# Optimization experiments

Measured on AMD Instinct MI355X. Metric: run time of the kernel, lower is better.

## Reference

```python
import jax, jax.numpy as jnp
import numpy as np

D = 2048
N = 4096
HEAD = 2
DH = D // HEAD


def setup_inputs() -> dict:
    key = jax.random.key(0)
    ks = jax.random.split(key, 7)
    s = 0.02  # realistic init scale for weights
    x = jax.random.normal(ks[0], (1, N, D), jnp.float32)
    Wq1 = jax.random.normal(ks[1], (DH, DH), jnp.float32) * s
    Wq2 = jax.random.normal(ks[2], (DH, DH), jnp.float32) * s
    Wk1 = jax.random.normal(ks[3], (DH, DH), jnp.float32) * s
    Wk2 = jax.random.normal(ks[4], (DH, DH), jnp.float32) * s
    Wv1 = jax.random.normal(ks[5], (DH, DH), jnp.float32) * s
    Wv2 = jax.random.normal(ks[6], (DH, DH), jnp.float32) * s
    return {"x": x, "Wq1": Wq1, "Wq2": Wq2, "Wk1": Wk1, "Wk2": Wk2,
            "Wv1": Wv1, "Wv2": Wv2}


def _head(xh, Wq, Wk, Wv):
    # xh: [1, N, Dh]; Linear applies in @ W^T (no bias)
    q = (xh @ Wq.T)[0]                      # [N, Dh]
    k = (xh @ Wk.T)[0]                      # [N, Dh] (k reshaped to 2D in torch)
    v = (xh @ Wv.T)[0]                      # [N, Dh]
    # QK_T linear with weight dynamically set to k (detached in torch):
    Sc = q @ jax.lax.stop_gradient(k).T     # [N, N]
    # Sc_V linear on v^T with weight set to Sc (detached in torch):
    Sc = jax.lax.stop_gradient(Sc)
    return v.T @ Sc.T                       # [Dh, N]  == (Sc @ v)^T


def reference(x, Wq1, Wq2, Wk1, Wk2, Wv1, Wv2):
    Dh = Wq1.shape[0]
    x1, x2 = x[..., :Dh], x[..., Dh:]       # torch.chunk(x, 2, dim=2)
    o1 = _head(x1, Wq1, Wk1, Wv1)           # [Dh, N]
    o2 = _head(x2, Wq2, Wk2, Wv2)           # [Dh, N]
    out = jnp.concatenate([o1, o2], axis=0).T  # transpose(-2,-1).squeeze -> [N, D]
    return out
```

## Files before the change

kernel.cpp:

```cpp
#include <hip/hip_runtime.h>
#include <hip/hip_bf16.h>


using bf16 = __hip_bfloat16;
typedef __attribute__((ext_vector_type(8))) __bf16 bf16x8;
typedef __attribute__((ext_vector_type(8))) unsigned short u16x8;
typedef __attribute__((ext_vector_type(4))) float f32x4;

#define M1 (1024 * 1024)

struct GB {
    const bf16* A[20];
    const bf16* B[20];
    void*       C[20];
    int lda[20];
    int ldb[20];
};

__device__ __forceinline__ void gload_lds16(const void* g, void* l) {
    __builtin_amdgcn_global_load_lds(
        (const __attribute__((address_space(1))) void*)g,
        (__attribute__((address_space(3))) void*)l, 16, 0, 0);
}

template<int N>
__device__ __forceinline__ void waitv() {
    if constexpr (N == 4)      asm volatile("s_waitcnt vmcnt(4)" ::: "memory");
    else if constexpr (N == 3) asm volatile("s_waitcnt vmcnt(3)" ::: "memory");
    else                       asm volatile("s_waitcnt vmcnt(0)" ::: "memory");
}

template<int BM_, int BN_, typename OUT_T>
__global__ __launch_bounds__(256, 4)
void gemm_bt_pa(GB g, int Ksub, int ldc)
{
    const int gx = gridDim.x, gy = gridDim.y;
    const int nwg = gx * gy * gridDim.z;
    const int orig = blockIdx.x + gx * (blockIdx.y + gy * blockIdx.z);
    const int cpx = nwg >> 3;
    const int wg = (orig & 7) * cpx + (orig >> 3);
    const int bx = wg % gx;
    const int by = (wg / gx) % gy;
    const int bz = wg / (gx * gy);

    const bf16* __restrict__ A = g.A[bz];
    const bf16* __restrict__ B = g.B[bz];
    OUT_T* __restrict__ C = (OUT_T*)g.C[bz];
    const int lda = g.lda[bz];
    const int ldb = g.ldb[bz];

    constexpr int STAGE_SH = 2 * (BM_ + BN_) * 32;
    constexpr int EPI_SH   = BM_ * BN_ * (int)sizeof(OUT_T) / 2;
    constexpr int SMEM_SH  = STAGE_SH > EPI_SH ? STAGE_SH : EPI_SH;
    __shared__ __align__(16) unsigned short smem[SMEM_SH];
    auto As = (unsigned short(*)[BM_ * 32])smem;
    auto Bs = (unsigned short(*)[BN_ * 32])(smem + 2 * BM_ * 32);

    constexpr int MI = BM_ / 32;
    constexpr int NI = BN_ / 32;
    constexpr int NLOADS = (BM_ + BN_) / 64;

    const int tid  = threadIdx.x;
    const int lane = tid & 63;
    const int wave = tid >> 6;
    const int wm   = wave >> 1;
    const int wn   = wave & 1;

    const int m0 = by * BM_;
    const int n0 = bx * BN_;

    const int fr = lane & 15;
    const int kg = lane >> 4;

    const int srow = tid >> 2;
    const int scol = (tid & 3) * 8;

    auto stage = [&](int buf, int kt) {
        #pragma unroll
        for (int r = 0; r < BM_ / 64; ++r)
            gload_lds16(A + (size_t)(m0 + r * 64 + srow) * lda + (kt + scol),
                        &As[buf][(r * 64 + srow) * 32 + scol]);
        #pragma unroll
        for (int r = 0; r < BN_ / 64; ++r)
            gload_lds16(B + (size_t)(n0 + r * 64 + srow) * ldb + (kt + scol),
                        &Bs[buf][(r * 64 + srow) * 32 + scol]);
    };

    f32x4 acc[MI][NI];
    #pragma unroll
    for (int i = 0; i < MI; ++i)
        #pragma unroll
        for (int j = 0; j < NI; ++j)
            acc[i][j] = {0.f, 0.f, 0.f, 0.f};

    const int niter = Ksub >> 5;
    int cur = 0;
    stage(0, 0);

    for (int it = 0; it < niter; ++it) {
        if (it + 1 < niter) {
            stage(cur ^ 1, (it + 1) << 5);
            waitv<NLOADS>();
        } else {
            waitv<0>();
        }
        __builtin_amdgcn_s_barrier();
        __builtin_amdgcn_sched_barrier(0);

        bf16x8 afrag[MI], bfrag[NI];
        #pragma unroll
        for (int mi = 0; mi < MI; ++mi)
            afrag[mi] = *(const bf16x8*)&As[cur][(wm * (BM_ / 2) + mi * 16 + fr) * 32 + kg * 8];
        #pragma unroll
        for (int ni = 0; ni < NI; ++ni)
            bfrag[ni] = *(const bf16x8*)&Bs[cur][(wn * (BN_ / 2) + ni * 16 + fr) * 32 + kg * 8];

        #pragma unroll
        for (int mi = 0; mi < MI; ++mi)
            #pragma unroll
            for (int ni = 0; ni < NI; ++ni)
                acc[mi][ni] = __builtin_amdgcn_mfma_f32_16x16x32_bf16(
                    afrag[mi], bfrag[ni], acc[mi][ni], 0, 0, 0);

        __builtin_amdgcn_sched_barrier(0);
        __builtin_amdgcn_s_barrier();
        __builtin_amdgcn_sched_barrier(0);
        cur ^= 1;
    }

    if constexpr (sizeof(OUT_T) == 2) {
        #pragma unroll
        for (int mi = 0; mi < MI; ++mi)
            #pragma unroll
            for (int ni = 0; ni < NI; ++ni) {
                const int c = wn * (BN_ / 2) + ni * 16 + fr;
                #pragma unroll
                for (int j = 0; j < 4; ++j) {
                    const int r = wm * (BM_ / 2) + mi * 16 + kg * 4 + j;
                    bf16 h = __float2bfloat16(acc[mi][ni][j]);
                    smem[r * BN_ + c] = *(unsigned short*)&h;
                }
            }
        __syncthreads();
        constexpr int V = (BM_ * BN_) / 2048;
        #pragma unroll
        for (int v = 0; v < V; ++v) {
            const int off = v * 2048 + tid * 8;
            const int r = off / BN_;
            const int c = off % BN_;
            *(u16x8*)((unsigned short*)C + (size_t)(m0 + r) * ldc + n0 + c) =
                *(const u16x8*)&smem[off];
        }
    } else {
        float* fs = (float*)smem;
        #pragma unroll
        for (int mi = 0; mi < MI; ++mi)
            #pragma unroll
            for (int ni = 0; ni < NI; ++ni) {
                const int c = wn * (BN_ / 2) + ni * 16 + fr;
                #pragma unroll
                for (int j = 0; j < 4; ++j) {
                    const int r = wm * (BM_ / 2) + mi * 16 + kg * 4 + j;
                    fs[r * BN_ + c] = acc[mi][ni][j];
                }
            }
        __syncthreads();
        constexpr int V = (BM_ * BN_) / 1024;
        #pragma unroll
        for (int v = 0; v < V; ++v) {
            const int off = v * 1024 + tid * 4;
            const int r = off / BN_;
            const int c = off % BN_;
            *(float4*)((float*)C + (size_t)(m0 + r) * ldc + n0 + c) =
                *(const float4*)&fs[off];
        }
    }
}


__device__ __forceinline__ ushort4 cvt4(float4 v) {
    ushort4 o; bf16 h;
    h = __float2bfloat16(v.x); o.x = *(unsigned short*)&h;
    h = __float2bfloat16(v.y); o.y = *(unsigned short*)&h;
    h = __float2bfloat16(v.z); o.z = *(unsigned short*)&h;
    h = __float2bfloat16(v.w); o.w = *(unsigned short*)&h;
    return o;
}

struct PrepArgs {
    const float* x;
    const float* w[4];
    const float* wv[2];
    bf16* xb;
    bf16* xt;
    bf16* wdst;
};

__device__ void xpose64(const float* __restrict__ src, int ldsrc,
                        int r0, int c0,
                        bf16* __restrict__ dstS, int ldS,
                        bf16* __restrict__ dstT, int ldT,
                        float (*tile)[65], int t)
{
    const int tr  = t >> 4;
    const int tc4 = (t & 15) * 4;
    #pragma unroll
    for (int ph = 0; ph < 4; ++ph) {
        const int row = ph * 16 + tr;
        float4 v = *(const float4*)(src + (size_t)(r0 + row) * ldsrc + c0 + tc4);
        tile[row][tc4 + 0] = v.x;
        tile[row][tc4 + 1] = v.y;
        tile[row][tc4 + 2] = v.z;
        tile[row][tc4 + 3] = v.w;
        if (dstS)
            *(ushort4*)((unsigned short*)dstS + (size_t)(r0 + row) * ldS + c0 + tc4) = cvt4(v);
    }
    __syncthreads();
    #pragma unroll
    for (int ph = 0; ph < 4; ++ph) {
        const int crow = ph * 16 + tr;
        float4 v = {tile[tc4 + 0][crow], tile[tc4 + 1][crow],
                    tile[tc4 + 2][crow], tile[tc4 + 3][crow]};
        *(ushort4*)((unsigned short*)dstT + (size_t)(c0 + crow) * ldT + r0 + tc4) = cvt4(v);
    }
}

__global__ void prep(PrepArgs p)
{
    __shared__ float tile[64][65];
    const int b = blockIdx.x;
    const int t = threadIdx.x;

    if (b < 2048) {
        const int n0 = (b & 63) * 64;
        const int c0 = (b >> 6) * 64;
        xpose64(p.x, 2048, n0, c0, p.xb, 2048, p.xt, 4096, tile, t);
    } else if (b < 3072) {
        const int i = b - 2048;
        const int mat = i >> 8;
        const int tl  = i & 255;
        const int r0 = (tl & 15) * 64;
        const int c0 = (tl >> 4) * 64;
        xpose64(p.w[mat], 1024, r0, c0, nullptr, 0,
                p.wdst + (size_t)mat * M1, 1024, tile, t);
    } else {
        const int i = b - 3072;
        const int mat = i >> 9;
        const int blk = i & 511;
        const size_t off = (size_t)blk * 2048 + t * 8;
        float4 v0 = *(const float4*)(p.wv[mat] + off);
        float4 v1 = *(const float4*)(p.wv[mat] + off + 4);
        unsigned short* d = (unsigned short*)p.wdst + (size_t)(4 + mat) * M1 + off;
        *(ushort4*)d       = cvt4(v0);
        *(ushort4*)(d + 4) = cvt4(v1);
    }
}


__device__ __forceinline__ void reduce_slices(const unsigned short* src,
                                              unsigned short* dst,
                                              int h, int r, int nslice)
{
    float acc[8] = {0, 0, 0, 0, 0, 0, 0, 0};
    for (int s = 0; s < nslice; ++s) {
        u16x8 v = *(const u16x8*)(src + ((size_t)(h * nslice + s) << 20) + r);
        #pragma unroll
        for (int j = 0; j < 8; ++j)
            acc[j] += __uint_as_float(((unsigned)v[j]) << 16);
    }
    u16x8 o;
    #pragma unroll
    for (int j = 0; j < 8; ++j) {
        bf16 hh = __float2bfloat16(acc[j]);
        o[j] = *(unsigned short*)&hh;
    }
    *(u16x8*)(dst + ((size_t)h << 20) + r) = o;
}

__global__ void reduce_GM(const unsigned short* Gp, const unsigned short* Mp,
                          unsigned short* Gd, unsigned short* Md)
{
    const int b = blockIdx.x, t = threadIdx.x;
    if (b < 1024) {
        const int e = (b * 256 + t) * 8;
        reduce_slices(Gp, Gd, e >> 20, e & (M1 - 1), 8);
    } else {
        const int e = ((b - 1024) * 256 + t) * 8;
        reduce_slices(Mp, Md, e >> 20, e & (M1 - 1), 2);
    }
}

__global__ void reduce_4(const unsigned short* Sp, unsigned short* Dd)
{
    const int e = (blockIdx.x * 256 + threadIdx.x) * 8;
    reduce_slices(Sp, Dd, e >> 20, e & (M1 - 1), 4);
}


extern "C" void kernel_launch(void* const* d_in, const int* in_sizes, int n_in,
                              void* d_out, int out_size, void* d_ws, size_t ws_size,
                              hipStream_t stream)
{
    bf16* xb   = (bf16*)d_ws;
    bf16* xt   = xb + 8 * M1;
    bf16* wdst = xt + 8 * M1;
    bf16* Mp   = wdst + 6 * M1;
    bf16* Mb   = Mp + 4 * M1;
    bf16* Gb   = Mb + 2 * M1;
    bf16* Ytb  = Gb + 2 * M1;
    bf16* Utb  = Ytb + 2 * M1;

    bf16* scr = (bf16*)d_out;

    PrepArgs pa;
    pa.x = (const float*)d_in[0];
    pa.w[0] = (const float*)d_in[1];  pa.w[1] = (const float*)d_in[2];
    pa.w[2] = (const float*)d_in[3];  pa.w[3] = (const float*)d_in[4];
    pa.wv[0] = (const float*)d_in[5]; pa.wv[1] = (const float*)d_in[6];
    pa.xb = xb; pa.xt = xt; pa.wdst = wdst;
    prep<<<4096, 256, 0, stream>>>(pa);

    GB g;

    for (int z = 0; z < 16; ++z) {
        const int h = z >> 3, s = z & 7;
        g.A[z] = xt + (size_t)h * 4 * M1 + s * 512;  g.lda[z] = 4096;
        g.B[z] = g.A[z];                             g.ldb[z] = 4096;
        g.C[z] = (bf16*)scr + (size_t)z * M1;
    }
    for (int z = 16; z < 20; ++z) {
        const int j = z - 16, h = j >> 1, s = j & 1;
        g.A[z] = wdst + (size_t)h * M1 + s * 512;           g.lda[z] = 1024;
        g.B[z] = wdst + (size_t)(2 + h) * M1 + s * 512;     g.ldb[z] = 1024;
        g.C[z] = Mp + (size_t)j * M1;
    }
    gemm_bt_pa<128, 128, bf16><<<dim3(8, 8, 20), 256, 0, stream>>>(g, 512, 1024);

    reduce_GM<<<2048, 256, 0, stream>>>((const unsigned short*)scr, (const unsigned short*)Mp,
                                        (unsigned short*)Gb, (unsigned short*)Mb);

    for (int z = 0; z < 8; ++z) {
        const int h = z >> 2, s = z & 3;
        g.A[z] = Mb + (size_t)h * M1 + s * 256;  g.lda[z] = 1024;
        g.B[z] = Gb + (size_t)h * M1 + s * 256;  g.ldb[z] = 1024;
        g.C[z] = (bf16*)scr + (size_t)z * M1;
    }
    gemm_bt_pa<128, 128, bf16><<<dim3(8, 8, 8), 256, 0, stream>>>(g, 256, 1024);

    reduce_4<<<1024, 256, 0, stream>>>((const unsigned short*)scr, (unsigned short*)Ytb);

    for (int z = 0; z < 8; ++z) {
        const int h = z >> 2, s = z & 3;
        g.A[z] = wdst + (size_t)(4 + h) * M1 + s * 256;  g.lda[z] = 1024;
        g.B[z] = Ytb + (size_t)h * M1 + s * 256;         g.ldb[z] = 1024;
        g.C[z] = (bf16*)scr + (size_t)z * M1;
    }
    gemm_bt_pa<128, 128, bf16><<<dim3(8, 8, 8), 256, 0, stream>>>(g, 256, 1024);

    reduce_4<<<1024, 256, 0, stream>>>((const unsigned short*)scr, (unsigned short*)Utb);

    for (int z = 0; z < 2; ++z) {
        g.A[z] = xb + (size_t)z * 1024;   g.lda[z] = 2048;
        g.B[z] = Utb + (size_t)z * M1;    g.ldb[z] = 1024;
        g.C[z] = (float*)d_out + (size_t)z * 1024;
    }
    gemm_bt_pa<128, 64, float><<<dim3(16, 32, 2), 256, 0, stream>>>(g, 1024, 2048);
}
```

Measured before the change: 124.3 us.

## Compute only upper-triangular tiles of symmetric Gram matrix and mirror in reduction

The Gram matrix G = X^T X per head is symmetric, so the first batched GEMM now computes only the 36 upper-triangular 128x128 tiles per split-K slice instead of all 64. The Wq·Wk product tiles are packed into the same launch as a second branch. The reduction kernel sums the compact tile slices and writes each off-diagonal tile twice, once transposed, which removes close to half of the Gram GEMM work and partial-sum traffic. In exchange, the mirrored writes are scattered element stores with poor coalescing, and the triangle index is decoded with a small loop.

```diff
diff --git a/kernel.cpp b/kernel.cpp
--- a/kernel.cpp
+++ b/kernel.cpp
@@ -10,11 +10,11 @@
 #define M1 (1024 * 1024)
 
 struct GB {
-    const bf16* A[20];
-    const bf16* B[20];
-    void*       C[20];
-    int lda[20];
-    int ldb[20];
+    const bf16* A[8];
+    const bf16* B[8];
+    void*       C[8];
+    int lda[8];
+    int ldb[8];
 };
 
 __device__ __forceinline__ void gload_lds16(const void* g, void* l) {
@@ -31,28 +31,13 @@
 }
 
 template<int BM_, int BN_, typename OUT_T>
-__global__ __launch_bounds__(256, 4)
-void gemm_bt_pa(GB g, int Ksub, int ldc)
-{
-    const int gx = gridDim.x, gy = gridDim.y;
-    const int nwg = gx * gy * gridDim.z;
-    const int orig = blockIdx.x + gx * (blockIdx.y + gy * blockIdx.z);
-    const int cpx = nwg >> 3;
-    const int wg = (orig & 7) * cpx + (orig >> 3);
-    const int bx = wg % gx;
-    const int by = (wg / gx) % gy;
-    const int bz = wg / (gx * gy);
-
-    const bf16* __restrict__ A = g.A[bz];
-    const bf16* __restrict__ B = g.B[bz];
-    OUT_T* __restrict__ C = (OUT_T*)g.C[bz];
-    const int lda = g.lda[bz];
-    const int ldb = g.ldb[bz];
-
-    constexpr int STAGE_SH = 2 * (BM_ + BN_) * 32;
-    constexpr int EPI_SH   = BM_ * BN_ * (int)sizeof(OUT_T) / 2;
-    constexpr int SMEM_SH  = STAGE_SH > EPI_SH ? STAGE_SH : EPI_SH;
-    __shared__ __align__(16) unsigned short smem[SMEM_SH];
+__device__ __forceinline__ void gemm_core(
+    const bf16* __restrict__ A, int lda,
+    const bf16* __restrict__ B, int ldb,
+    OUT_T* __restrict__ C, int ldc,
+    int m0, int n0, int Ksub,
+    unsigned short* smem, int tid)
+{
     auto As = (unsigned short(*)[BM_ * 32])smem;
     auto Bs = (unsigned short(*)[BN_ * 32])(smem + 2 * BM_ * 32);
 
@@ -60,18 +45,12 @@
     constexpr int NI = BN_ / 32;
     constexpr int NLOADS = (BM_ + BN_) / 64;
 
-    const int tid  = threadIdx.x;
     const int lane = tid & 63;
     const int wave = tid >> 6;
     const int wm   = wave >> 1;
     const int wn   = wave & 1;
-
-    const int m0 = by * BM_;
-    const int n0 = bx * BN_;
-
     const int fr = lane & 15;
     const int kg = lane >> 4;
-
     const int srow = tid >> 2;
     const int scol = (tid & 3) * 8;
 
@@ -174,6 +153,73 @@
             *(float4*)((float*)C + (size_t)(m0 + r) * ldc + n0 + c) =
                 *(const float4*)&fs[off];
         }
+    }
+}
+
+template<int BM_, int BN_, typename OUT_T>
+__global__ __launch_bounds__(256, 4)
+void gemm_bt_pa(GB g, int Ksub, int ldc)
+{
+    constexpr int STAGE_SH = 2 * (BM_ + BN_) * 32;
+    constexpr int EPI_SH   = BM_ * BN_ * (int)sizeof(OUT_T) / 2;
+    constexpr int SMEM_SH  = STAGE_SH > EPI_SH ? STAGE_SH : EPI_SH;
+    __shared__ __align__(16) unsigned short smem[SMEM_SH];
+
+    const int gx = gridDim.x, gy = gridDim.y;
+    const int nwg = gx * gy * gridDim.z;
+    const int orig = blockIdx.x + gx * (blockIdx.y + gy * blockIdx.z);
+    const int cpx = nwg >> 3;
+    const int wg = (orig & 7) * cpx + (orig >> 3);
+    const int bx = wg % gx;
+    const int by = (wg / gx) % gy;
+    const int bz = wg / (gx * gy);
+
+    gemm_core<BM_, BN_, OUT_T>(g.A[bz], g.lda[bz], g.B[bz], g.ldb[bz],
+                               (OUT_T*)g.C[bz], ldc,
+                               by * BM_, bx * BN_, Ksub,
+                               smem, threadIdx.x);
+}
+
+struct B1Args {
+    const bf16* xt;
+    const bf16* wdst;
+    bf16* Gp;
+    bf16* Mp;
+};
+
+__global__ __launch_bounds__(256, 4)
+void b1_kernel(B1Args a)
+{
+    __shared__ __align__(16) unsigned short smem[16384];
+
+    const int nwg = 832;
+    const int orig = blockIdx.x + 52 * blockIdx.z;
+    const int cpx = nwg >> 3;
+    const int wg = (orig & 7) * cpx + (orig >> 3);
+    const int bx = wg % 52;
+    const int bz = wg / 52;
+
+    if (bx < 36) {
+        const int h = bz >> 3, s = bz & 7;
+        int ti = 0, rem = bx;
+        while (rem >= 8 - ti) { rem -= 8 - ti; ++ti; }
+        const int tj = ti + rem;
+        const bf16* A = a.xt + (size_t)(h * 1024 + ti * 128) * 4096 + s * 512;
+        const bf16* B = a.xt + (size_t)(h * 1024 + tj * 128) * 4096 + s * 512;
+        bf16* C = a.Gp + ((size_t)bz * 36 + bx) * 16384;
+        gemm_core<128, 128, bf16>(A, 4096, B, 4096, C, 128, 0, 0, 512,
+                                  smem, threadIdx.x);
+    } else {
+        const int combo = bz & 3;
+        const int h = combo >> 1, s = combo & 1;
+        const int tile = (bz >> 2) * 16 + (bx - 36);
+        const int m0 = (tile >> 3) * 128;
+        const int n0 = (tile & 7) * 128;
+        const bf16* A = a.wdst + (size_t)h * M1 + s * 512;
+        const bf16* B = a.wdst + (size_t)(2 + h) * M1 + s * 512;
+        bf16* C = a.Mp + (size_t)combo * M1;
+        gemm_core<128, 128, bf16>(A, 1024, B, 1024, C, 1024, m0, n0, 512,
+                                  smem, threadIdx.x);
     }
 }
 
@@ -281,11 +327,41 @@
                           unsigned short* Gd, unsigned short* Md)
 {
     const int b = blockIdx.x, t = threadIdx.x;
-    if (b < 1024) {
-        const int e = (b * 256 + t) * 8;
-        reduce_slices(Gp, Gd, e >> 20, e & (M1 - 1), 8);
+    if (b < 576) {
+        const int h    = b / 288;
+        const int rem  = b - h * 288;
+        const int tile = rem >> 3;
+        const int blk  = rem & 7;
+        int ti = 0, trem = tile;
+        while (trem >= 8 - ti) { trem -= 8 - ti; ++ti; }
+        const int tj = ti + trem;
+
+        const int e  = blk * 2048 + t * 8;
+        const int r  = e >> 7;
+        const int c0 = e & 127;
+
+        float acc[8] = {0, 0, 0, 0, 0, 0, 0, 0};
+        for (int s = 0; s < 8; ++s) {
+            u16x8 v = *(const u16x8*)(Gp + ((size_t)(h * 8 + s) * 36 + tile) * 16384 + e);
+            #pragma unroll
+            for (int j = 0; j < 8; ++j)
+                acc[j] += __uint_as_float(((unsigned)v[j]) << 16);
+        }
+        u16x8 o;
+        #pragma unroll
+        for (int j = 0; j < 8; ++j) {
+            bf16 hh = __float2bfloat16(acc[j]);
+            o[j] = *(unsigned short*)&hh;
+        }
+        unsigned short* G = Gd + (size_t)h * M1;
+        *(u16x8*)(G + (size_t)(ti * 128 + r) * 1024 + tj * 128 + c0) = o;
+        if (ti != tj) {
+            #pragma unroll
+            for (int j = 0; j < 8; ++j)
+                G[(size_t)(tj * 128 + c0 + j) * 1024 + ti * 128 + r] = o[j];
+        }
     } else {
-        const int e = ((b - 1024) * 256 + t) * 8;
+        const int e = ((b - 576) * 256 + t) * 8;
         reduce_slices(Mp, Md, e >> 20, e & (M1 - 1), 2);
     }
 }
@@ -320,24 +396,15 @@
     pa.xb = xb; pa.xt = xt; pa.wdst = wdst;
     prep<<<4096, 256, 0, stream>>>(pa);
 
+    B1Args b1;
+    b1.xt = xt; b1.wdst = wdst; b1.Gp = scr; b1.Mp = Mp;
+    b1_kernel<<<dim3(52, 1, 16), 256, 0, stream>>>(b1);
+
+    reduce_GM<<<1600, 256, 0, stream>>>((const unsigned short*)scr,
+                                        (const unsigned short*)Mp,
+                                        (unsigned short*)Gb, (unsigned short*)Mb);
+
     GB g;
-
-    for (int z = 0; z < 16; ++z) {
-        const int h = z >> 3, s = z & 7;
-        g.A[z] = xt + (size_t)h * 4 * M1 + s * 512;  g.lda[z] = 4096;
-        g.B[z] = g.A[z];                             g.ldb[z] = 4096;
-        g.C[z] = (bf16*)scr + (size_t)z * M1;
-    }
-    for (int z = 16; z < 20; ++z) {
-        const int j = z - 16, h = j >> 1, s = j & 1;
-        g.A[z] = wdst + (size_t)h * M1 + s * 512;           g.lda[z] = 1024;
-        g.B[z] = wdst + (size_t)(2 + h) * M1 + s * 512;     g.ldb[z] = 1024;
-        g.C[z] = Mp + (size_t)j * M1;
-    }
-    gemm_bt_pa<128, 128, bf16><<<dim3(8, 8, 20), 256, 0, stream>>>(g, 512, 1024);
-
-    reduce_GM<<<2048, 256, 0, stream>>>((const unsigned short*)scr, (const unsigned short*)Mp,
-                                        (unsigned short*)Gb, (unsigned short*)Mb);
 
     for (int z = 0; z < 8; ++z) {
         const int h = z >> 2, s = z & 3;
```

After: 119.9 us. -3.5%, faster.
